# Performance work log

Measured on AMD Instinct MI355X. Metric: run time of the kernel, lower is better.

The kernel has to match this reference:

```python
import jax, jax.numpy as jnp
import numpy as np

# dims (match init_kwargs)
L, D, H, K = 8, 384, 6, 64            # layers, hidden, rwkv heads, rwkv head dim
DI, MH, HD, DS, CK = 768, 12, 64, 64, 4  # mamba: d_inner, heads, head_dim, d_state, conv kernel
V, B, T = 32000, 1, 1024


def _rms(x, w, eps=1e-6):
    return w * x * jax.lax.rsqrt(jnp.mean(x * x, axis=-1, keepdims=True) + eps)


def _rwkv6(xn, Wr, Wk, Wv, Wg, Ww, w_bias, u, gn_w, gn_b, Wo):
    # RWKV6: data-dependent diagonal-decay linear attention
    Bb, Tt, Dd = xn.shape
    proj = lambda W: (xn @ W).reshape(Bb, Tt, H, K)
    r, k, v = proj(Wr), proj(Wk), proj(Wv)
    g = xn @ Wg                                        # [B,T,D]
    w = (xn @ Ww + w_bias).reshape(Bb, Tt, H, K)
    decay = jnp.exp(-jnp.exp(w))                       # in (0,1)

    def step(S, inp):                                  # S: [B,H,K,K] (key x value)
        r_t, k_t, v_t, d_t = inp                       # each [B,H,K]
        kv = k_t[..., :, None] * v_t[..., None, :]     # [B,H,K,K]
        o = jnp.einsum('bhk,bhkv->bhv', r_t, S + u[None, :, :, None] * kv)
        S = d_t[..., None] * S + kv
        return S, o

    tm = lambda a: jnp.moveaxis(a, 1, 0)               # time-major
    S0 = jnp.zeros((Bb, H, K, K), xn.dtype)
    _, o = jax.lax.scan(step, S0, (tm(r), tm(k), tm(v), tm(decay)))
    o = jnp.moveaxis(o, 0, 1)                          # [B,T,H,K]
    # per-head GroupNorm
    mu = jnp.mean(o, -1, keepdims=True)
    var = jnp.var(o, -1, keepdims=True)
    o = (o - mu) * jax.lax.rsqrt(var + 1e-5) * gn_w.reshape(H, K) + gn_b.reshape(H, K)
    o = o.reshape(Bb, Tt, Dd) * jax.nn.silu(g)
    return o @ Wo


def _mamba2(xn, W_in, conv_w, conv_b, dt_bias, A_log, Dp, mn_w, W_out):
    # Mamba2: selective scan with scalar A per head
    Bb, Tt, Dd = xn.shape
    zxbcdt = xn @ W_in                                 # [B,T, 2*DI + 2*DS + MH]
    z = zxbcdt[..., :DI]
    xBC = zxbcdt[..., DI:DI + DI + 2 * DS]
    dt = jax.nn.softplus(zxbcdt[..., -MH:] + dt_bias)  # [B,T,MH]
    # causal depthwise conv1d, kernel CK
    xp = jnp.pad(xBC, ((0, 0), (CK - 1, 0), (0, 0)))
    xBC = sum(xp[:, j:j + Tt, :] * conv_w[:, j] for j in range(CK)) + conv_b
    xBC = jax.nn.silu(xBC)
    xs = xBC[..., :DI].reshape(Bb, Tt, MH, HD)
    Bm = xBC[..., DI:DI + DS]                          # [B,T,DS]
    Cm = xBC[..., DI + DS:]                            # [B,T,DS]
    A = -jnp.exp(A_log)                                # [MH]

    def step(S, inp):                                  # S: [B,MH,HD,DS]
        x_t, B_t, C_t, dt_t = inp                      # [B,MH,HD],[B,DS],[B,DS],[B,MH]
        dA = jnp.exp(dt_t * A)                         # [B,MH]
        S = dA[..., None, None] * S + (dt_t[..., None] * x_t)[..., None] * B_t[:, None, None, :]
        y = jnp.einsum('bhps,bs->bhp', S, C_t) + Dp[None, :, None] * x_t
        return S, y

    tm = lambda a: jnp.moveaxis(a, 1, 0)
    S0 = jnp.zeros((Bb, MH, HD, DS), xn.dtype)
    _, y = jax.lax.scan(step, S0, (tm(xs), tm(Bm), tm(Cm), tm(dt)))
    y = jnp.moveaxis(y, 0, 1).reshape(Bb, Tt, DI)
    y = _rms(y * jax.nn.silu(z), mn_w)                 # gated RMSNorm
    return y @ W_out


def _forward(x, embed, ln_w, Wr, Wk, Wv, Wg, Ww, w_bias, u, gn_w, gn_b, Wo,
             W_in, conv_w, conv_b, dt_bias, A_log, Dp, mn_w, W_out,
             gw, gb, ffn_ln_w, ffn_w1, ffn_w2, ln_out_w):
    h = jnp.take(embed, x, axis=0)                     # [B,T,D]
    for i in range(L):
        xn = _rms(h, ln_w[i])
        o_r = _rwkv6(xn, Wr[i], Wk[i], Wv[i], Wg[i], Ww[i], w_bias[i], u[i], gn_w[i], gn_b[i], Wo[i])
        o_m = _mamba2(xn, W_in[i], conv_w[i], conv_b[i], dt_bias[i], A_log[i], Dp[i], mn_w[i], W_out[i])
        gate = jax.nn.sigmoid(jnp.concatenate([o_r, o_m], -1) @ gw[i] + gb[i])  # [B,T,1]
        h = h + gate * o_r + (1.0 - gate) * o_m
        hn = _rms(h, ffn_ln_w[i])
        h = h + jax.nn.gelu(hn @ ffn_w1[i], approximate=False) @ ffn_w2[i]
    h = _rms(h, ln_out_w)
    return h @ embed.T                                 # tied head -> [B,T,V]


def setup_inputs() -> dict:
    key = jax.random.key(0)
    ks = iter(jax.random.split(key, 32))
    n = lambda shape, s=0.02: jax.random.normal(next(ks), shape, jnp.float32) * s
    d = {}
    d['x'] = jax.random.randint(next(ks), (B, T), 0, V)
    d['embed'] = n((V, D))
    d['ln_w'] = jnp.ones((L, D), jnp.float32)
    d['Wr'] = n((L, D, D)); d['Wk'] = n((L, D, D)); d['Wv'] = n((L, D, D))
    d['Wg'] = n((L, D, D)); d['Ww'] = n((L, D, D))
    d['w_bias'] = n((L, D), 0.5)
    d['u'] = n((L, H, K), 0.5)
    d['gn_w'] = jnp.ones((L, D), jnp.float32)
    d['gn_b'] = jnp.zeros((L, D), jnp.float32)
    d['Wo'] = n((L, D, D))
    d['W_in'] = n((L, D, 2 * DI + 2 * DS + MH))
    d['conv_w'] = n((L, DI + 2 * DS, CK), 0.2)
    d['conv_b'] = jnp.zeros((L, DI + 2 * DS), jnp.float32)
    d['dt_bias'] = jax.random.uniform(next(ks), (L, MH), jnp.float32, -4.0, -1.0)
    d['A_log'] = jnp.log(jax.random.uniform(next(ks), (L, MH), jnp.float32, 1.0, 16.0))
    d['Dp'] = jnp.ones((L, MH), jnp.float32)
    d['mn_w'] = jnp.ones((L, DI), jnp.float32)
    d['W_out'] = n((L, DI, D))
    d['gw'] = n((L, 2 * D, 1), 0.01)
    d['gb'] = jnp.full((L, 1), float(np.log(0.3 / 0.7)), jnp.float32)
    d['ffn_ln_w'] = jnp.ones((L, D), jnp.float32)
    d['ffn_w1'] = n((L, D, 4 * D))
    d['ffn_w2'] = n((L, 4 * D, D))
    d['ln_out_w'] = jnp.ones((D,), jnp.float32)
    return d


def reference(x, embed, ln_w, Wr, Wk, Wv, Wg, Ww, w_bias, u, gn_w, gn_b, Wo,
              W_in, conv_w, conv_b, dt_bias, A_log, Dp, mn_w, W_out,
              gw, gb, ffn_ln_w, ffn_w1, ffn_w2, ln_out_w):
    return _forward(x, embed, ln_w, Wr, Wk, Wv, Wg, Ww, w_bias, u, gn_w, gn_b, Wo,
                    W_in, conv_w, conv_b, dt_bias, A_log, Dp, mn_w, W_out,
                    gw, gb, ffn_ln_w, ffn_w1, ffn_w2, ln_out_w)
```

## Files before the change

kernel.cpp:

```cpp
#include <hip/hip_runtime.h>
#include <math.h>

#define TT 1024
#define DD 384
#define NH 6
#define DI 768
#define MH 12
#define DS 64
#define NL 8
#define XDIM 1676
#define CONVC 896
#define NV 32000
#define PZS 3712
#define G_OFF 1152
#define W_OFF 1536
#define Z_OFF 1920
#define XBC_OFF 2688
#define DT_OFF 3584
#define CHK 32
#define NCH 32

typedef __attribute__((ext_vector_type(8))) short short8;
typedef __attribute__((ext_vector_type(4))) float f32x4;

__device__ __forceinline__ float siluf(float x) { return x / (1.f + expf(-x)); }
__device__ __forceinline__ float sigmoidf_(float x) { return 1.f / (1.f + expf(-x)); }
__device__ __forceinline__ float geluf(float x) {
  return 0.5f * x * (1.f + erff(x * 0.70710678118654752440f));
}
__device__ __forceinline__ unsigned short f2b(float x) {
  union { float f; unsigned int u; } v; v.f = x;
  unsigned int r = v.u + 0x7fffu + ((v.u >> 16) & 1u);
  return (unsigned short)(r >> 16);
}

#define GLDS(gp, lp) __builtin_amdgcn_global_load_lds( \
    (const __attribute__((address_space(1))) void*)(gp), \
    (__attribute__((address_space(3))) void*)(lp), 16, 0, 0)

template<int EPI>
__global__ __launch_bounds__(256) void gemm_bf16(
    const unsigned short* __restrict__ A, const unsigned short* __restrict__ Bt,
    float* __restrict__ C, unsigned short* __restrict__ Cb, int N, int K, int ldC)
{
  __shared__ unsigned short As[2048];
  __shared__ unsigned short Bs[2048];
  int tid = threadIdx.x;
  int wid = tid >> 6, lane = tid & 63;
  int m0 = blockIdx.y * 64, n0 = blockIdx.x * 64;
  int wr = wid >> 1, wc = wid & 1;
  int sr = tid >> 2;
  int scs = ((tid & 3) ^ ((sr >> 1) & 3)) * 8;
  const unsigned short* ga = A  + (size_t)(m0 + sr) * K + scs;
  const unsigned short* gb = Bt + (size_t)(n0 + sr) * K + scs;
  unsigned short* la = As + wid * 512;
  unsigned short* lb = Bs + wid * 512;
  int fr = lane & 15, fc = lane >> 4;
  f32x4 zz = {0.f, 0.f, 0.f, 0.f};
  f32x4 acc[2][2];
  acc[0][0] = zz; acc[0][1] = zz; acc[1][0] = zz; acc[1][1] = zz;

  int kper = K / (int)gridDim.z;
  int ks = blockIdx.z * kper, ke = ks + kper;
  for (int k0 = ks; k0 < ke; k0 += 32) {
    GLDS(ga + k0, la);
    GLDS(gb + k0, lb);
    __syncthreads();
    short8 af[2], bf[2];
#pragma unroll
    for (int mg = 0; mg < 2; ++mg) {
      int ar = wr * 32 + mg * 16 + fr;
      af[mg] = *reinterpret_cast<const short8*>(&As[ar * 32 + ((fc ^ ((ar >> 1) & 3)) * 8)]);
    }
#pragma unroll
    for (int ng = 0; ng < 2; ++ng) {
      int br = wc * 32 + ng * 16 + fr;
      bf[ng] = *reinterpret_cast<const short8*>(&Bs[br * 32 + ((fc ^ ((br >> 1) & 3)) * 8)]);
    }
#pragma unroll
    for (int mg = 0; mg < 2; ++mg)
#pragma unroll
      for (int ng = 0; ng < 2; ++ng)
        acc[mg][ng] = __builtin_amdgcn_mfma_f32_16x16x32_bf16(af[mg], bf[ng], acc[mg][ng], 0, 0, 0);
    __syncthreads();
  }
#pragma unroll
  for (int mg = 0; mg < 2; ++mg)
#pragma unroll
    for (int ng = 0; ng < 2; ++ng) {
      int col = n0 + wc * 32 + ng * 16 + fr;
      if (col < N) {
#pragma unroll
        for (int j = 0; j < 4; ++j) {
          int row = m0 + wr * 32 + mg * 16 + fc * 4 + j;
          if (EPI == 1)      Cb[(size_t)row * ldC + col] = f2b(geluf(acc[mg][ng][j]));
          else if (EPI == 3) atomicAdd(&C[(size_t)row * ldC + col], acc[mg][ng][j]);
          else               C[(size_t)row * ldC + col]  = acc[mg][ng][j];
        }
      }
    }
}

__global__ __launch_bounds__(256) void gemm_dual(
    const unsigned short* __restrict__ A0, const unsigned short* __restrict__ B0t,
    float* __restrict__ C0, int K0, int ld0, int nx0, int nb0,
    const unsigned short* __restrict__ A1, const unsigned short* __restrict__ B1t,
    float* __restrict__ C1, int K1, int ld1, int nx1)
{
  __shared__ unsigned short As[2048];
  __shared__ unsigned short Bs[2048];
  int b = blockIdx.x;
  const unsigned short *A, *Bt; float* C; int K, ldC, bx, by;
  if (b < nb0) { A = A0; Bt = B0t; C = C0; K = K0; ldC = ld0; bx = b % nx0; by = b / nx0; }
  else { b -= nb0; A = A1; Bt = B1t; C = C1; K = K1; ldC = ld1; bx = b % nx1; by = b / nx1; }
  int tid = threadIdx.x;
  int wid = tid >> 6, lane = tid & 63;
  int m0 = by * 64, n0 = bx * 64;
  int wr = wid >> 1, wc = wid & 1;
  int sr = tid >> 2;
  int scs = ((tid & 3) ^ ((sr >> 1) & 3)) * 8;
  const unsigned short* ga = A  + (size_t)(m0 + sr) * K + scs;
  const unsigned short* gb = Bt + (size_t)(n0 + sr) * K + scs;
  unsigned short* la = As + wid * 512;
  unsigned short* lb = Bs + wid * 512;
  int fr = lane & 15, fc = lane >> 4;
  f32x4 zz = {0.f, 0.f, 0.f, 0.f};
  f32x4 acc[2][2];
  acc[0][0] = zz; acc[0][1] = zz; acc[1][0] = zz; acc[1][1] = zz;
  for (int k0 = 0; k0 < K; k0 += 32) {
    GLDS(ga + k0, la);
    GLDS(gb + k0, lb);
    __syncthreads();
    short8 af[2], bf[2];
#pragma unroll
    for (int mg = 0; mg < 2; ++mg) {
      int ar = wr * 32 + mg * 16 + fr;
      af[mg] = *reinterpret_cast<const short8*>(&As[ar * 32 + ((fc ^ ((ar >> 1) & 3)) * 8)]);
    }
#pragma unroll
    for (int ng = 0; ng < 2; ++ng) {
      int br = wc * 32 + ng * 16 + fr;
      bf[ng] = *reinterpret_cast<const short8*>(&Bs[br * 32 + ((fc ^ ((br >> 1) & 3)) * 8)]);
    }
#pragma unroll
    for (int mg = 0; mg < 2; ++mg)
#pragma unroll
      for (int ng = 0; ng < 2; ++ng)
        acc[mg][ng] = __builtin_amdgcn_mfma_f32_16x16x32_bf16(af[mg], bf[ng], acc[mg][ng], 0, 0, 0);
    __syncthreads();
  }
#pragma unroll
  for (int mg = 0; mg < 2; ++mg)
#pragma unroll
    for (int ng = 0; ng < 2; ++ng) {
      int col = n0 + wc * 32 + ng * 16 + fr;
#pragma unroll
      for (int j = 0; j < 4; ++j) {
        int row = m0 + wr * 32 + mg * 16 + fc * 4 + j;
        C[(size_t)row * ldC + col] = acc[mg][ng][j];
      }
    }
}

__global__ __launch_bounds__(256) void gemm128(
    const unsigned short* __restrict__ A, const unsigned short* __restrict__ Bt,
    float* __restrict__ C, int N, int K, int ldC)
{
  __shared__ unsigned short As[4096];
  __shared__ unsigned short Bs[4096];
  int tid = threadIdx.x;
  int wid = tid >> 6, lane = tid & 63;
  int m0 = blockIdx.y * 128, n0 = blockIdx.x * 128;
  int wr = wid >> 1, wc = wid & 1;
  int r0 = tid >> 2;
  int scs = ((tid & 3) ^ ((r0 >> 1) & 3)) * 8;
  const unsigned short* ga0 = A  + (size_t)(m0 + r0) * K + scs;
  const unsigned short* gb0 = Bt + (size_t)(n0 + r0) * K + scs;
  const unsigned short* ga1 = ga0 + (size_t)64 * K;
  const unsigned short* gb1 = gb0 + (size_t)64 * K;
  unsigned short* la0 = As + wid * 512;
  unsigned short* lb0 = Bs + wid * 512;
  unsigned short* la1 = As + 2048 + wid * 512;
  unsigned short* lb1 = Bs + 2048 + wid * 512;
  int fr = lane & 15, fc = lane >> 4;
  f32x4 zz = {0.f, 0.f, 0.f, 0.f};
  f32x4 acc[4][4];
#pragma unroll
  for (int i = 0; i < 4; i++)
#pragma unroll
    for (int j = 0; j < 4; j++) acc[i][j] = zz;

  for (int k0 = 0; k0 < K; k0 += 32) {
    GLDS(ga0 + k0, la0);
    GLDS(gb0 + k0, lb0);
    GLDS(ga1 + k0, la1);
    GLDS(gb1 + k0, lb1);
    __syncthreads();
    short8 af[4], bf[4];
#pragma unroll
    for (int mg = 0; mg < 4; ++mg) {
      int ar = wr * 64 + mg * 16 + fr;
      af[mg] = *reinterpret_cast<const short8*>(&As[ar * 32 + ((fc ^ ((ar >> 1) & 3)) * 8)]);
    }
#pragma unroll
    for (int ng = 0; ng < 4; ++ng) {
      int br = wc * 64 + ng * 16 + fr;
      bf[ng] = *reinterpret_cast<const short8*>(&Bs[br * 32 + ((fc ^ ((br >> 1) & 3)) * 8)]);
    }
#pragma unroll
    for (int mg = 0; mg < 4; ++mg)
#pragma unroll
      for (int ng = 0; ng < 4; ++ng)
        acc[mg][ng] = __builtin_amdgcn_mfma_f32_16x16x32_bf16(af[mg], bf[ng], acc[mg][ng], 0, 0, 0);
    __syncthreads();
  }
#pragma unroll
  for (int mg = 0; mg < 4; ++mg)
#pragma unroll
    for (int ng = 0; ng < 4; ++ng) {
      int col = n0 + wc * 64 + ng * 16 + fr;
      if (col < N) {
#pragma unroll
        for (int j = 0; j < 4; ++j) {
          int row = m0 + wr * 64 + mg * 16 + fc * 4 + j;
          C[(size_t)row * ldC + col] = acc[mg][ng][j];
        }
      }
    }
}

__global__ __launch_bounds__(256) void transconv_kernel(
    const float* __restrict__ src, unsigned short* __restrict__ dst,
    int K, int N, int Npad, size_t srcStride, size_t dstStride)
{
  __shared__ float tile[32][33];
  src += (size_t)blockIdx.z * srcStride;
  dst += (size_t)blockIdx.z * dstStride;
  int k0 = blockIdx.y * 32, n0 = blockIdx.x * 32;
  int tx = threadIdx.x & 31, ty = threadIdx.x >> 5;
  for (int i = ty; i < 32; i += 8) {
    int k = k0 + i, n = n0 + tx;
    tile[i][tx] = (k < K && n < N) ? src[(size_t)k * N + n] : 0.f;
  }
  __syncthreads();
  for (int i = ty; i < 32; i += 8) {
    int n = n0 + i, k = k0 + tx;
    if (n < Npad && k < K) dst[(size_t)n * K + k] = f2b(tile[tx][i]);
  }
}

__global__ void conv_b16_kernel(const float* __restrict__ src, unsigned short* __restrict__ dst, int n)
{
  int idx = blockIdx.x * 256 + threadIdx.x;
  if (idx < n) dst[idx] = f2b(src[idx]);
}

__global__ void embed_kernel(const int* __restrict__ x, const float* __restrict__ embed,
                             float* __restrict__ h)
{
  int idx = blockIdx.x * 256 + threadIdx.x;
  if (idx < TT * DD) {
    int t = idx / DD, d = idx % DD;
    h[idx] = embed[(size_t)x[t] * DD + d];
  }
}

__global__ __launch_bounds__(256) void rms_kernel(const float* __restrict__ in,
                                                  const float* __restrict__ w,
                                                  unsigned short* __restrict__ out)
{
  int row = blockIdx.x * 4 + (threadIdx.x >> 6);
  int lane = threadIdx.x & 63;
  const float* r = in + (size_t)row * DD;
  float v[6]; float ss = 0.f;
#pragma unroll
  for (int j = 0; j < 6; ++j) { v[j] = r[lane + j * 64]; ss = fmaf(v[j], v[j], ss); }
#pragma unroll
  for (int s = 1; s < 64; s <<= 1) ss += __shfl_xor(ss, s);
  float scale = rsqrtf(ss * (1.f / DD) + 1e-6f);
#pragma unroll
  for (int j = 0; j < 6; ++j)
    out[(size_t)row * DD + lane + j * 64] = f2b(w[lane + j * 64] * v[j] * scale);
}

__global__ __launch_bounds__(256) void scanA_kernel(
    const float* __restrict__ PZ, const float* __restrict__ u, const float* __restrict__ wbias,
    float* __restrict__ so, float* __restrict__ rPb,
    float* __restrict__ MstR, float* __restrict__ DcR,
    const float* __restrict__ cw, const float* __restrict__ cbia,
    const float* __restrict__ dtbias,
    const float* __restrict__ Alog, const float* __restrict__ Dpw,
    float* __restrict__ yb, float* __restrict__ Ccb,
    float* __restrict__ MstM, float* __restrict__ DcM)
{
  __shared__ float smem[2 * 256 + 64];
  int b = blockIdx.x, tid = threadIdx.x;
  if (b < 192) {
    int h = b >> 5, c = b & 31;
    float* sbuf = smem; float* us = smem + 512;
    if (tid < 64) us[tid] = u[h * 64 + tid];
    int wv = tid >> 6, l = tid & 63;
    int vv = wv * 16 + (l & 15);
    int kc = l >> 4;
    int arr = tid >> 6, idx = tid & 63;
    int off = (arr == 0) ? 0 : (arr == 1) ? 384 : (arr == 2) ? W_OFF : 768;
    float wb = (arr == 2) ? wbias[h * 64 + idx] : 0.f;
    size_t base = (size_t)h * 64 + idx + off;
    int t0 = c * CHK;
    float S[16], Pc[16];
#pragma unroll
    for (int i = 0; i < 16; i++) { S[i] = 0.f; Pc[i] = 1.f; }
    float reg = PZ[(size_t)t0 * PZS + base];
    bool st = (wv == 0) && ((l & 15) == 0);
    for (int t = 0; t < CHK; ++t) {
      int tt = t0 + t;
      float* cb = sbuf + (t & 1) * 256;
      cb[arr * 64 + idx] = (arr == 2) ? expf(-expf(reg + wb)) : reg;
      if (t + 1 < CHK) reg = PZ[(size_t)(tt + 1) * PZS + base];
      __syncthreads();
      float vt = cb[192 + vv];
      float acc = 0.f;
      float rp[16];
#pragma unroll
      for (int i = 0; i < 16; ++i) {
        int kk = kc * 16 + i;
        float rv = cb[kk], kv = cb[64 + kk], dv = cb[128 + kk];
        rp[i] = rv * Pc[i];
        float kvv = kv * vt;
        acc = fmaf(rv, fmaf(us[kk], kvv, S[i]), acc);
        S[i] = fmaf(dv, S[i], kvv);
        Pc[i] *= dv;
      }
      acc += __shfl_xor(acc, 16);
      acc += __shfl_xor(acc, 32);
      if (l < 16) so[(size_t)tt * DD + h * 64 + vv] = acc;
      if (st) {
        float4* dst = (float4*)&rPb[(size_t)tt * DD + h * 64 + kc * 16];
        dst[0] = make_float4(rp[0], rp[1], rp[2], rp[3]);
        dst[1] = make_float4(rp[4], rp[5], rp[6], rp[7]);
        dst[2] = make_float4(rp[8], rp[9], rp[10], rp[11]);
        dst[3] = make_float4(rp[12], rp[13], rp[14], rp[15]);
      }
    }
    float* ms = MstR + (size_t)(h * NCH + c) * 4096;
    float4* msv = (float4*)&ms[vv * 64 + kc * 16];
    msv[0] = make_float4(S[0], S[1], S[2], S[3]);
    msv[1] = make_float4(S[4], S[5], S[6], S[7]);
    msv[2] = make_float4(S[8], S[9], S[10], S[11]);
    msv[3] = make_float4(S[12], S[13], S[14], S[15]);
    if (st) {
      float4* dd_ = (float4*)&DcR[(h * NCH + c) * 64 + kc * 16];
      dd_[0] = make_float4(Pc[0], Pc[1], Pc[2], Pc[3]);
      dd_[1] = make_float4(Pc[4], Pc[5], Pc[6], Pc[7]);
      dd_[2] = make_float4(Pc[8], Pc[9], Pc[10], Pc[11]);
      dd_[3] = make_float4(Pc[12], Pc[13], Pc[14], Pc[15]);
    }
  } else {
    int bb = b - 192;
    int hh = bb >> 5, c = bb & 31;
    float* sbuf = smem;
    int wv = tid >> 6, l = tid & 63;
    int p = wv * 16 + (l & 15);
    int sc = l >> 4;
    int arr = tid >> 6, idx = tid & 63;
    float A = -expf(Alog[hh]);
    float Dph = Dpw[hh];
    float dtbh = dtbias[hh];
    int t0 = c * CHK;
    float cw0 = 0.f, cw1 = 0.f, cw2 = 0.f, cw3 = 0.f, cbv = 0.f;
    float xw0 = 0.f, xw1 = 0.f, xw2 = 0.f, cur = 0.f;
    const float* xcol = nullptr;
    float reg = 0.f;
    if (arr < 3) {
      int ch = (arr == 0) ? (hh * 64 + idx) : (arr == 1) ? (DI + idx) : (DI + DS + idx);
      cw0 = cw[ch * 4 + 0]; cw1 = cw[ch * 4 + 1]; cw2 = cw[ch * 4 + 2]; cw3 = cw[ch * 4 + 3];
      cbv = cbia[ch];
      xcol = PZ + XBC_OFF + ch;
      xw0 = (t0 >= 3) ? xcol[(size_t)(t0 - 3) * PZS] : 0.f;
      xw1 = (t0 >= 2) ? xcol[(size_t)(t0 - 2) * PZS] : 0.f;
      xw2 = (t0 >= 1) ? xcol[(size_t)(t0 - 1) * PZS] : 0.f;
      cur = xcol[(size_t)t0 * PZS];
    } else {
      reg = PZ[(size_t)t0 * PZS + DT_OFF + hh];
    }
    float S[16]; float cdA = 1.f;
#pragma unroll
    for (int i = 0; i < 16; i++) S[i] = 0.f;
    bool st = (wv == 0) && ((l & 15) == 0);
    for (int t = 0; t < CHK; ++t) {
      int tt = t0 + t;
      float* cb = sbuf + (t & 1) * 256;
      if (arr < 3) {
        float cvv = fmaf(cw3, cur, fmaf(cw2, xw2, fmaf(cw1, xw1, fmaf(cw0, xw0, cbv))));
        cb[arr * 64 + idx] = siluf(cvv);
        float nx = (t + 1 < CHK) ? xcol[(size_t)(tt + 1) * PZS] : 0.f;
        xw0 = xw1; xw1 = xw2; xw2 = cur; cur = nx;
      } else {
        if (idx == 0) {
          float v = reg + dtbh;
          cb[192] = (v > 20.f) ? v : log1pf(expf(v));
        }
        if (t + 1 < CHK) reg = PZ[(size_t)(tt + 1) * PZS + DT_OFF + hh];
      }
      __syncthreads();
      float dt_ = cb[192];
      float dA = expf(dt_ * A);
      cdA *= dA;
      float xp = cb[p];
      float dtx = dt_ * xp;
      float acc = 0.f;
#pragma unroll
      for (int i = 0; i < 16; ++i) {
        int s = sc * 16 + i;
        S[i] = fmaf(dA, S[i], dtx * cb[64 + s]);
        acc = fmaf(S[i], cb[128 + s], acc);
      }
      acc += __shfl_xor(acc, 16);
      acc += __shfl_xor(acc, 32);
      if (l < 16) yb[(size_t)tt * DI + hh * 64 + p] = fmaf(Dph, xp, acc);
      if (st) {
        float4* dst = (float4*)&Ccb[(size_t)tt * DI + hh * 64 + sc * 16];
#pragma unroll
        for (int j4 = 0; j4 < 4; ++j4)
          dst[j4] = make_float4(cdA * cb[128 + sc * 16 + j4 * 4 + 0],
                                cdA * cb[128 + sc * 16 + j4 * 4 + 1],
                                cdA * cb[128 + sc * 16 + j4 * 4 + 2],
                                cdA * cb[128 + sc * 16 + j4 * 4 + 3]);
      }
    }
    float* ms = MstM + (size_t)(hh * NCH + c) * 4096;
    float4* msv = (float4*)&ms[p * 64 + sc * 16];
    msv[0] = make_float4(S[0], S[1], S[2], S[3]);
    msv[1] = make_float4(S[4], S[5], S[6], S[7]);
    msv[2] = make_float4(S[8], S[9], S[10], S[11]);
    msv[3] = make_float4(S[12], S[13], S[14], S[15]);
    if (tid == 0) DcM[hh * NCH + c] = cdA;
  }
}

__global__ __launch_bounds__(256) void combine_kernel(
    const float* __restrict__ MstR, const float* __restrict__ DcR, float* __restrict__ S0R,
    const float* __restrict__ MstM, const float* __restrict__ DcM, float* __restrict__ S0M)
{
  int b = blockIdx.x, tid = threadIdx.x;
  if (b < 96) {
    int h = b >> 4, sub = b & 15;
    int ei = sub * 256 + tid;
    int k = ei & 63;
    float S = 0.f;
#pragma unroll
    for (int c = 0; c < NCH; ++c) {
      size_t base = (size_t)(h * NCH + c) * 4096;
      float m = MstR[base + ei];
      float dD = DcR[(h * NCH + c) * 64 + k];
      S0R[base + ei] = S;
      S = fmaf(dD, S, m);
    }
  } else {
    int bb = b - 96;
    int hh = bb >> 4, sub = bb & 15;
    int ei = sub * 256 + tid;
    float S = 0.f;
#pragma unroll
    for (int c = 0; c < NCH; ++c) {
      size_t base = (size_t)(hh * NCH + c) * 4096;
      float m = MstM[base + ei];
      float dD = DcM[hh * NCH + c];
      S0M[base + ei] = S;
      S = fmaf(dD, S, m);
    }
  }
}

__global__ __launch_bounds__(256) void corr_kernel(
    const float* __restrict__ S0R, const float* __restrict__ rPb, const float* __restrict__ so,
    const float* __restrict__ S0M, const float* __restrict__ Ccb, float* __restrict__ yb,
    const float* __restrict__ PZ, const float* __restrict__ gnw, const float* __restrict__ gnb,
    unsigned short* __restrict__ gob)
{
  __shared__ float S0l[64 * 68];
  __shared__ float Rl[CHK * 68];
  int b = blockIdx.x, tid = threadIdx.x;
  const float* s0g; const float* rg; int ostride, obase, t0;
  bool rwkv = (b < 192);
  int h;
  if (rwkv) {
    h = b >> 5; int c = b & 31; t0 = c * CHK;
    s0g = S0R + (size_t)(h * NCH + c) * 4096;
    rg = rPb; obase = h * 64; ostride = DD;
  } else {
    int bb = b - 192; h = bb >> 5; int c = bb & 31; t0 = c * CHK;
    s0g = S0M + (size_t)(h * NCH + c) * 4096;
    rg = Ccb; obase = h * 64; ostride = DI;
  }
  for (int gi = tid; gi < 4096; gi += 256)
    S0l[(gi & 63) * 68 + (gi >> 6)] = s0g[gi];
  {
    int t = tid >> 3, q = (tid & 7) * 8;
    const float4* src = (const float4*)&rg[(size_t)(t0 + t) * ostride + obase + q];
    float4* dst = (float4*)&Rl[t * 68 + q];
    dst[0] = src[0]; dst[1] = src[1];
  }
  __syncthreads();
  int t = tid >> 3, q = (tid & 7) * 8;
  float acc[8];
#pragma unroll
  for (int j = 0; j < 8; j++) acc[j] = 0.f;
  for (int k = 0; k < 64; ++k) {
    float rv = Rl[t * 68 + k];
    const float4* sp = (const float4*)&S0l[k * 68 + q];
    float4 s0 = sp[0], s1 = sp[1];
    acc[0] = fmaf(rv, s0.x, acc[0]);
    acc[1] = fmaf(rv, s0.y, acc[1]);
    acc[2] = fmaf(rv, s0.z, acc[2]);
    acc[3] = fmaf(rv, s0.w, acc[3]);
    acc[4] = fmaf(rv, s1.x, acc[4]);
    acc[5] = fmaf(rv, s1.y, acc[5]);
    acc[6] = fmaf(rv, s1.z, acc[6]);
    acc[7] = fmaf(rv, s1.w, acc[7]);
  }
  if (!rwkv) {
    float4* op = (float4*)&yb[(size_t)(t0 + t) * DI + obase + q];
    float4 c0 = op[0], c1 = op[1];
    c0.x += acc[0]; c0.y += acc[1]; c0.z += acc[2]; c0.w += acc[3];
    c1.x += acc[4]; c1.y += acc[5]; c1.z += acc[6]; c1.w += acc[7];
    op[0] = c0; op[1] = c1;
  } else {
    float ov[8];
    const float4* sp = (const float4*)&so[(size_t)(t0 + t) * DD + obase + q];
    float4 s0 = sp[0], s1 = sp[1];
    ov[0] = s0.x + acc[0]; ov[1] = s0.y + acc[1]; ov[2] = s0.z + acc[2]; ov[3] = s0.w + acc[3];
    ov[4] = s1.x + acc[4]; ov[5] = s1.y + acc[5]; ov[6] = s1.z + acc[6]; ov[7] = s1.w + acc[7];
    float m_ = 0.f;
#pragma unroll
    for (int j = 0; j < 8; j++) m_ += ov[j];
    m_ += __shfl_xor(m_, 1); m_ += __shfl_xor(m_, 2); m_ += __shfl_xor(m_, 4);
    float mu = m_ * (1.f / 64.f);
    float vv = 0.f;
#pragma unroll
    for (int j = 0; j < 8; j++) { float d = ov[j] - mu; vv = fmaf(d, d, vv); }
    vv += __shfl_xor(vv, 1); vv += __shfl_xor(vv, 2); vv += __shfl_xor(vv, 4);
    float rstd = rsqrtf(vv * (1.f / 64.f) + 1e-5f);
#pragma unroll
    for (int j = 0; j < 8; j++) {
      int d = obase + q + j;
      float gv = PZ[(size_t)(t0 + t) * PZS + G_OFF + d];
      float o = fmaf((ov[j] - mu) * rstd, gnw[d], gnb[d]) * siluf(gv);
      gob[(size_t)(t0 + t) * DD + d] = f2b(o);
    }
  }
}

__global__ __launch_bounds__(256) void mamba_norm_kernel(const float* __restrict__ yb,
    const float* __restrict__ PZ, const float* __restrict__ mnw, unsigned short* __restrict__ out)
{
  int row = blockIdx.x * 4 + (threadIdx.x >> 6);
  int lane = threadIdx.x & 63;
  float v[12]; float ss = 0.f;
#pragma unroll
  for (int j = 0; j < 12; ++j) {
    int c = lane + j * 64;
    float z = PZ[(size_t)row * PZS + Z_OFF + c];
    float t = yb[(size_t)row * DI + c] * siluf(z);
    v[j] = t; ss = fmaf(t, t, ss);
  }
#pragma unroll
  for (int s = 1; s < 64; s <<= 1) ss += __shfl_xor(ss, s);
  float scale = rsqrtf(ss * (1.f / DI) + 1e-6f);
#pragma unroll
  for (int j = 0; j < 12; ++j) {
    int c = lane + j * 64;
    out[(size_t)row * DI + c] = f2b(v[j] * scale * mnw[c]);
  }
}

__global__ __launch_bounds__(256) void gate_rms_kernel(const float* __restrict__ orb,
    const float* __restrict__ omb, const float* __restrict__ gw,
    const float* __restrict__ gb, const float* __restrict__ flnw,
    float* __restrict__ h, unsigned short* __restrict__ xnb)
{
  int row = blockIdx.x * 4 + (threadIdx.x >> 6);
  int lane = threadIdx.x & 63;
  float a[6], bq[6]; float ss = 0.f;
#pragma unroll
  for (int j = 0; j < 6; ++j) {
    int c = lane + j * 64;
    a[j] = orb[(size_t)row * DD + c]; bq[j] = omb[(size_t)row * DD + c];
    ss += a[j] * gw[c] + bq[j] * gw[DD + c];
  }
#pragma unroll
  for (int s = 1; s < 64; s <<= 1) ss += __shfl_xor(ss, s);
  float gate = sigmoidf_(ss + gb[0]);
  float hn[6]; float ss2 = 0.f;
#pragma unroll
  for (int j = 0; j < 6; ++j) {
    int c = lane + j * 64;
    size_t ix = (size_t)row * DD + c;
    hn[j] = h[ix] + gate * a[j] + (1.f - gate) * bq[j];
    h[ix] = hn[j];
    ss2 = fmaf(hn[j], hn[j], ss2);
  }
#pragma unroll
  for (int s = 1; s < 64; s <<= 1) ss2 += __shfl_xor(ss2, s);
  float scale = rsqrtf(ss2 * (1.f / DD) + 1e-6f);
#pragma unroll
  for (int j = 0; j < 6; ++j) {
    int c = lane + j * 64;
    xnb[(size_t)row * DD + c] = f2b(flnw[c] * hn[j] * scale);
  }
}

extern "C" void kernel_launch(void* const* d_in, const int* in_sizes, int n_in,
                              void* d_out, int out_size, void* d_ws, size_t ws_size,
                              hipStream_t stream)
{
  const int*   x        = (const int*)  d_in[0];
  const float* embed    = (const float*)d_in[1];
  const float* ln_w     = (const float*)d_in[2];
  const float* Wr       = (const float*)d_in[3];
  const float* Wk       = (const float*)d_in[4];
  const float* Wv       = (const float*)d_in[5];
  const float* Wg       = (const float*)d_in[6];
  const float* Ww       = (const float*)d_in[7];
  const float* w_bias   = (const float*)d_in[8];
  const float* u        = (const float*)d_in[9];
  const float* gn_w     = (const float*)d_in[10];
  const float* gn_b     = (const float*)d_in[11];
  const float* Wo       = (const float*)d_in[12];
  const float* W_in     = (const float*)d_in[13];
  const float* conv_w   = (const float*)d_in[14];
  const float* conv_b   = (const float*)d_in[15];
  const float* dt_bias  = (const float*)d_in[16];
  const float* A_log    = (const float*)d_in[17];
  const float* Dp       = (const float*)d_in[18];
  const float* mn_w     = (const float*)d_in[19];
  const float* W_out    = (const float*)d_in[20];
  const float* gw       = (const float*)d_in[21];
  const float* gb       = (const float*)d_in[22];
  const float* ffn_ln_w = (const float*)d_in[23];
  const float* ffn_w1   = (const float*)d_in[24];
  const float* ffn_w2   = (const float*)d_in[25];
  const float* ln_out_w = (const float*)d_in[26];

  char* base = (char*)d_ws;
  size_t off = 0;
  auto alloc = [&](size_t bytes) { off = (off + 255) & ~(size_t)255; void* p = base + off; off += bytes; return p; };

  float* h    = (float*)alloc((size_t)TT * DD * 4);
  float* PZ   = (float*)alloc((size_t)TT * PZS * 4);
  float* yb   = (float*)alloc((size_t)TT * DI * 4);
  float* so   = (float*)alloc((size_t)TT * DD * 4);
  float* orb  = (float*)alloc((size_t)TT * DD * 4);
  float* omb  = (float*)alloc((size_t)TT * DD * 4);
  float* rPb  = (float*)alloc((size_t)TT * DD * 4);
  float* Ccb  = (float*)alloc((size_t)TT * DI * 4);
  float* MstR = (float*)alloc((size_t)NH * NCH * 4096 * 4);
  float* DcR  = (float*)alloc((size_t)NH * NCH * 64 * 4);
  float* S0R  = (float*)alloc((size_t)NH * NCH * 4096 * 4);
  float* MstM = (float*)alloc((size_t)MH * NCH * 4096 * 4);
  float* DcM  = (float*)alloc((size_t)MH * NCH * 4);
  float* S0M  = (float*)alloc((size_t)MH * NCH * 4096 * 4);
  unsigned short* xnb = (unsigned short*)alloc((size_t)TT * DD * 2);
  unsigned short* gob = (unsigned short*)alloc((size_t)TT * DD * 2);
  unsigned short* ynb = (unsigned short*)alloc((size_t)TT * DI * 2);
  unsigned short* fhb = (unsigned short*)alloc((size_t)TT * 1536 * 2);
  unsigned short* WallT = (unsigned short*)alloc((size_t)NL * PZS * 384 * 2);
  unsigned short* WoT   = (unsigned short*)alloc((size_t)NL * 384 * 384 * 2);
  unsigned short* WoutT = (unsigned short*)alloc((size_t)NL * 384 * 768 * 2);
  unsigned short* F1T   = (unsigned short*)alloc((size_t)NL * 1536 * 384 * 2);
  unsigned short* F2T   = (unsigned short*)alloc((size_t)NL * 384 * 1536 * 2);
  unsigned short* embB  = (unsigned short*)alloc((size_t)NV * DD * 2);
  (void)ws_size; (void)in_sizes; (void)n_in; (void)out_size;

  dim3 blk(256);
  int gTD = (TT * DD + 255) / 256;

  const float* Wrkvgw[5] = {Wr, Wk, Wv, Wg, Ww};
  for (int j = 0; j < 5; ++j)
    transconv_kernel<<<dim3(12, 12, 8), blk, 0, stream>>>(
        Wrkvgw[j], WallT + (size_t)j * 384 * 384, 384, 384, 384,
        (size_t)384 * 384, (size_t)PZS * 384);
  transconv_kernel<<<dim3(56, 12, 8), blk, 0, stream>>>(
      W_in, WallT + (size_t)1920 * 384, 384, XDIM, 1792,
      (size_t)384 * XDIM, (size_t)PZS * 384);
  transconv_kernel<<<dim3(12, 12, 8), blk, 0, stream>>>(
      Wo, WoT, 384, 384, 384, (size_t)384 * 384, (size_t)384 * 384);
  transconv_kernel<<<dim3(12, 24, 8), blk, 0, stream>>>(
      W_out, WoutT, 768, 384, 384, (size_t)768 * 384, (size_t)384 * 768);
  transconv_kernel<<<dim3(48, 12, 8), blk, 0, stream>>>(
      ffn_w1, F1T, 384, 1536, 1536, (size_t)384 * 1536, (size_t)1536 * 384);
  transconv_kernel<<<dim3(12, 48, 8), blk, 0, stream>>>(
      ffn_w2, F2T, 1536, 384, 384, (size_t)1536 * 384, (size_t)384 * 1536);
  conv_b16_kernel<<<(NV * DD + 255) / 256, blk, 0, stream>>>(embed, embB, NV * DD);

  embed_kernel<<<gTD, blk, 0, stream>>>(x, embed, h);

  for (int i = 0; i < NL; ++i) {
    rms_kernel<<<256, blk, 0, stream>>>(h, ln_w + (size_t)i * DD, xnb);

    gemm_bf16<0><<<dim3(58, 16), blk, 0, stream>>>(
        xnb, WallT + (size_t)i * PZS * 384, PZ, nullptr, PZS, 384, PZS);

    scanA_kernel<<<576, blk, 0, stream>>>(PZ, u + (size_t)i * NH * 64, w_bias + (size_t)i * DD,
                                          so, rPb, MstR, DcR,
                                          conv_w + (size_t)i * CONVC * 4, conv_b + (size_t)i * CONVC,
                                          dt_bias + (size_t)i * MH,
                                          A_log + (size_t)i * MH, Dp + (size_t)i * MH,
                                          yb, Ccb, MstM, DcM);
    combine_kernel<<<288, blk, 0, stream>>>(MstR, DcR, S0R, MstM, DcM, S0M);
    corr_kernel<<<576, blk, 0, stream>>>(S0R, rPb, so, S0M, Ccb, yb,
                                         PZ, gn_w + (size_t)i * DD, gn_b + (size_t)i * DD, gob);

    mamba_norm_kernel<<<256, blk, 0, stream>>>(yb, PZ, mn_w + (size_t)i * DI, ynb);

    gemm_dual<<<192, blk, 0, stream>>>(
        gob, WoT + (size_t)i * 384 * 384, orb, 384, DD, 6, 96,
        ynb, WoutT + (size_t)i * 384 * 768, omb, 768, DD, 6);

    gate_rms_kernel<<<256, blk, 0, stream>>>(orb, omb, gw + (size_t)i * 2 * DD, gb + i,
                                             ffn_ln_w + (size_t)i * DD, h, xnb);

    gemm_bf16<1><<<dim3(24, 16), blk, 0, stream>>>(
        xnb, F1T + (size_t)i * 1536 * 384, nullptr, fhb, 1536, 384, 1536);
    gemm_bf16<3><<<dim3(6, 16, 4), blk, 0, stream>>>(
        fhb, F2T + (size_t)i * 384 * 1536, h, nullptr, DD, 1536, DD);
  }

  rms_kernel<<<256, blk, 0, stream>>>(h, ln_out_w, xnb);
  gemm128<<<dim3(250, 8), blk, 0, stream>>>(
      xnb, embB, (float*)d_out, NV, 384, NV);
}
```

Measured before the change: 980.6 us.

## Double GEMM K-step, batch weight transposes, fold chunk-state combine into correction

All three GEMM kernels now stage 64-wide K tiles (two MFMA sub-steps per barrier) with an 8-way XOR swizzle, halving the number of loop iterations and barriers. The ten weight transpose/convert launches are merged into a single table-driven launch. The separate combine kernel is removed: each correction block recomputes its own prefix chunk state in registers by looping over prior chunks. This drops one launch per layer and two scratch buffers, but later chunks redo up to 31 chunk-state reads, so the correction kernel does redundant global traffic.

```diff
diff --git a/kernel.cpp b/kernel.cpp
--- a/kernel.cpp
+++ b/kernel.cpp
@@ -43,16 +43,16 @@
     const unsigned short* __restrict__ A, const unsigned short* __restrict__ Bt,
     float* __restrict__ C, unsigned short* __restrict__ Cb, int N, int K, int ldC)
 {
-  __shared__ unsigned short As[2048];
-  __shared__ unsigned short Bs[2048];
+  __shared__ unsigned short As[4096];
+  __shared__ unsigned short Bs[4096];
   int tid = threadIdx.x;
   int wid = tid >> 6, lane = tid & 63;
   int m0 = blockIdx.y * 64, n0 = blockIdx.x * 64;
   int wr = wid >> 1, wc = wid & 1;
-  int sr = tid >> 2;
-  int scs = ((tid & 3) ^ ((sr >> 1) & 3)) * 8;
-  const unsigned short* ga = A  + (size_t)(m0 + sr) * K + scs;
-  const unsigned short* gb = Bt + (size_t)(n0 + sr) * K + scs;
+  int r0 = tid >> 3, ch = tid & 7;
+  int scs = (ch ^ (r0 & 7)) * 8;
+  const unsigned short* ga = A  + (size_t)(m0 + r0) * K + scs;
+  const unsigned short* gb = Bt + (size_t)(n0 + r0) * K + scs;
   unsigned short* la = As + wid * 512;
   unsigned short* lb = Bs + wid * 512;
   int fr = lane & 15, fc = lane >> 4;
@@ -62,26 +62,32 @@
 
   int kper = K / (int)gridDim.z;
   int ks = blockIdx.z * kper, ke = ks + kper;
-  for (int k0 = ks; k0 < ke; k0 += 32) {
+  size_t row32 = (size_t)32 * K;
+  for (int k0 = ks; k0 < ke; k0 += 64) {
     GLDS(ga + k0, la);
+    GLDS(ga + k0 + row32, la + 2048);
     GLDS(gb + k0, lb);
+    GLDS(gb + k0 + row32, lb + 2048);
     __syncthreads();
-    short8 af[2], bf[2];
-#pragma unroll
-    for (int mg = 0; mg < 2; ++mg) {
-      int ar = wr * 32 + mg * 16 + fr;
-      af[mg] = *reinterpret_cast<const short8*>(&As[ar * 32 + ((fc ^ ((ar >> 1) & 3)) * 8)]);
-    }
-#pragma unroll
-    for (int ng = 0; ng < 2; ++ng) {
-      int br = wc * 32 + ng * 16 + fr;
-      bf[ng] = *reinterpret_cast<const short8*>(&Bs[br * 32 + ((fc ^ ((br >> 1) & 3)) * 8)]);
-    }
-#pragma unroll
-    for (int mg = 0; mg < 2; ++mg)
-#pragma unroll
-      for (int ng = 0; ng < 2; ++ng)
-        acc[mg][ng] = __builtin_amdgcn_mfma_f32_16x16x32_bf16(af[mg], bf[ng], acc[mg][ng], 0, 0, 0);
+#pragma unroll
+    for (int kh = 0; kh < 2; ++kh) {
+      short8 af[2], bf[2];
+#pragma unroll
+      for (int mg = 0; mg < 2; ++mg) {
+        int ar = wr * 32 + mg * 16 + fr;
+        af[mg] = *reinterpret_cast<const short8*>(&As[ar * 64 + (((kh * 4 + fc) ^ (ar & 7)) * 8)]);
+      }
+#pragma unroll
+      for (int ng = 0; ng < 2; ++ng) {
+        int br = wc * 32 + ng * 16 + fr;
+        bf[ng] = *reinterpret_cast<const short8*>(&Bs[br * 64 + (((kh * 4 + fc) ^ (br & 7)) * 8)]);
+      }
+#pragma unroll
+      for (int mg = 0; mg < 2; ++mg)
+#pragma unroll
+        for (int ng = 0; ng < 2; ++ng)
+          acc[mg][ng] = __builtin_amdgcn_mfma_f32_16x16x32_bf16(af[mg], bf[ng], acc[mg][ng], 0, 0, 0);
+    }
     __syncthreads();
   }
 #pragma unroll
@@ -107,8 +113,8 @@
     const unsigned short* __restrict__ A1, const unsigned short* __restrict__ B1t,
     float* __restrict__ C1, int K1, int ld1, int nx1)
 {
-  __shared__ unsigned short As[2048];
-  __shared__ unsigned short Bs[2048];
+  __shared__ unsigned short As[4096];
+  __shared__ unsigned short Bs[4096];
   int b = blockIdx.x;
   const unsigned short *A, *Bt; float* C; int K, ldC, bx, by;
   if (b < nb0) { A = A0; Bt = B0t; C = C0; K = K0; ldC = ld0; bx = b % nx0; by = b / nx0; }
@@ -117,36 +123,42 @@
   int wid = tid >> 6, lane = tid & 63;
   int m0 = by * 64, n0 = bx * 64;
   int wr = wid >> 1, wc = wid & 1;
-  int sr = tid >> 2;
-  int scs = ((tid & 3) ^ ((sr >> 1) & 3)) * 8;
-  const unsigned short* ga = A  + (size_t)(m0 + sr) * K + scs;
-  const unsigned short* gb = Bt + (size_t)(n0 + sr) * K + scs;
+  int r0 = tid >> 3, ch = tid & 7;
+  int scs = (ch ^ (r0 & 7)) * 8;
+  const unsigned short* ga = A  + (size_t)(m0 + r0) * K + scs;
+  const unsigned short* gb = Bt + (size_t)(n0 + r0) * K + scs;
   unsigned short* la = As + wid * 512;
   unsigned short* lb = Bs + wid * 512;
   int fr = lane & 15, fc = lane >> 4;
   f32x4 zz = {0.f, 0.f, 0.f, 0.f};
   f32x4 acc[2][2];
   acc[0][0] = zz; acc[0][1] = zz; acc[1][0] = zz; acc[1][1] = zz;
-  for (int k0 = 0; k0 < K; k0 += 32) {
+  size_t row32 = (size_t)32 * K;
+  for (int k0 = 0; k0 < K; k0 += 64) {
     GLDS(ga + k0, la);
+    GLDS(ga + k0 + row32, la + 2048);
     GLDS(gb + k0, lb);
+    GLDS(gb + k0 + row32, lb + 2048);
     __syncthreads();
-    short8 af[2], bf[2];
-#pragma unroll
-    for (int mg = 0; mg < 2; ++mg) {
-      int ar = wr * 32 + mg * 16 + fr;
-      af[mg] = *reinterpret_cast<const short8*>(&As[ar * 32 + ((fc ^ ((ar >> 1) & 3)) * 8)]);
-    }
-#pragma unroll
-    for (int ng = 0; ng < 2; ++ng) {
-      int br = wc * 32 + ng * 16 + fr;
-      bf[ng] = *reinterpret_cast<const short8*>(&Bs[br * 32 + ((fc ^ ((br >> 1) & 3)) * 8)]);
-    }
-#pragma unroll
-    for (int mg = 0; mg < 2; ++mg)
-#pragma unroll
-      for (int ng = 0; ng < 2; ++ng)
-        acc[mg][ng] = __builtin_amdgcn_mfma_f32_16x16x32_bf16(af[mg], bf[ng], acc[mg][ng], 0, 0, 0);
+#pragma unroll
+    for (int kh = 0; kh < 2; ++kh) {
+      short8 af[2], bf[2];
+#pragma unroll
+      for (int mg = 0; mg < 2; ++mg) {
+        int ar = wr * 32 + mg * 16 + fr;
+        af[mg] = *reinterpret_cast<const short8*>(&As[ar * 64 + (((kh * 4 + fc) ^ (ar & 7)) * 8)]);
+      }
+#pragma unroll
+      for (int ng = 0; ng < 2; ++ng) {
+        int br = wc * 32 + ng * 16 + fr;
+        bf[ng] = *reinterpret_cast<const short8*>(&Bs[br * 64 + (((kh * 4 + fc) ^ (br & 7)) * 8)]);
+      }
+#pragma unroll
+      for (int mg = 0; mg < 2; ++mg)
+#pragma unroll
+        for (int ng = 0; ng < 2; ++ng)
+          acc[mg][ng] = __builtin_amdgcn_mfma_f32_16x16x32_bf16(af[mg], bf[ng], acc[mg][ng], 0, 0, 0);
+    }
     __syncthreads();
   }
 #pragma unroll
@@ -166,22 +178,16 @@
     const unsigned short* __restrict__ A, const unsigned short* __restrict__ Bt,
     float* __restrict__ C, int N, int K, int ldC)
 {
-  __shared__ unsigned short As[4096];
-  __shared__ unsigned short Bs[4096];
+  __shared__ unsigned short As[8192];
+  __shared__ unsigned short Bs[8192];
   int tid = threadIdx.x;
   int wid = tid >> 6, lane = tid & 63;
   int m0 = blockIdx.y * 128, n0 = blockIdx.x * 128;
   int wr = wid >> 1, wc = wid & 1;
-  int r0 = tid >> 2;
-  int scs = ((tid & 3) ^ ((r0 >> 1) & 3)) * 8;
-  const unsigned short* ga0 = A  + (size_t)(m0 + r0) * K + scs;
-  const unsigned short* gb0 = Bt + (size_t)(n0 + r0) * K + scs;
-  const unsigned short* ga1 = ga0 + (size_t)64 * K;
-  const unsigned short* gb1 = gb0 + (size_t)64 * K;
-  unsigned short* la0 = As + wid * 512;
-  unsigned short* lb0 = Bs + wid * 512;
-  unsigned short* la1 = As + 2048 + wid * 512;
-  unsigned short* lb1 = Bs + 2048 + wid * 512;
+  int r0 = tid >> 3, ch = tid & 7;
+  int scs = (ch ^ (r0 & 7)) * 8;
+  const unsigned short* ga = A  + (size_t)(m0 + r0) * K + scs;
+  const unsigned short* gb = Bt + (size_t)(n0 + r0) * K + scs;
   int fr = lane & 15, fc = lane >> 4;
   f32x4 zz = {0.f, 0.f, 0.f, 0.f};
   f32x4 acc[4][4];
@@ -190,28 +196,33 @@
 #pragma unroll
     for (int j = 0; j < 4; j++) acc[i][j] = zz;
 
-  for (int k0 = 0; k0 < K; k0 += 32) {
-    GLDS(ga0 + k0, la0);
-    GLDS(gb0 + k0, lb0);
-    GLDS(ga1 + k0, la1);
-    GLDS(gb1 + k0, lb1);
+  size_t row32 = (size_t)32 * K;
+  for (int k0 = 0; k0 < K; k0 += 64) {
+#pragma unroll
+    for (int i = 0; i < 4; ++i) {
+      GLDS(ga + k0 + i * row32, As + i * 2048 + wid * 512);
+      GLDS(gb + k0 + i * row32, Bs + i * 2048 + wid * 512);
+    }
     __syncthreads();
-    short8 af[4], bf[4];
-#pragma unroll
-    for (int mg = 0; mg < 4; ++mg) {
-      int ar = wr * 64 + mg * 16 + fr;
-      af[mg] = *reinterpret_cast<const short8*>(&As[ar * 32 + ((fc ^ ((ar >> 1) & 3)) * 8)]);
-    }
-#pragma unroll
-    for (int ng = 0; ng < 4; ++ng) {
-      int br = wc * 64 + ng * 16 + fr;
-      bf[ng] = *reinterpret_cast<const short8*>(&Bs[br * 32 + ((fc ^ ((br >> 1) & 3)) * 8)]);
-    }
-#pragma unroll
-    for (int mg = 0; mg < 4; ++mg)
-#pragma unroll
-      for (int ng = 0; ng < 4; ++ng)
-        acc[mg][ng] = __builtin_amdgcn_mfma_f32_16x16x32_bf16(af[mg], bf[ng], acc[mg][ng], 0, 0, 0);
+#pragma unroll
+    for (int kh = 0; kh < 2; ++kh) {
+      short8 af[4], bf[4];
+#pragma unroll
+      for (int mg = 0; mg < 4; ++mg) {
+        int ar = wr * 64 + mg * 16 + fr;
+        af[mg] = *reinterpret_cast<const short8*>(&As[ar * 64 + (((kh * 4 + fc) ^ (ar & 7)) * 8)]);
+      }
+#pragma unroll
+      for (int ng = 0; ng < 4; ++ng) {
+        int br = wc * 64 + ng * 16 + fr;
+        bf[ng] = *reinterpret_cast<const short8*>(&Bs[br * 64 + (((kh * 4 + fc) ^ (br & 7)) * 8)]);
+      }
+#pragma unroll
+      for (int mg = 0; mg < 4; ++mg)
+#pragma unroll
+        for (int ng = 0; ng < 4; ++ng)
+          acc[mg][ng] = __builtin_amdgcn_mfma_f32_16x16x32_bf16(af[mg], bf[ng], acc[mg][ng], 0, 0, 0);
+    }
     __syncthreads();
   }
 #pragma unroll
@@ -229,23 +240,31 @@
     }
 }
 
-__global__ __launch_bounds__(256) void transconv_kernel(
-    const float* __restrict__ src, unsigned short* __restrict__ dst,
-    int K, int N, int Npad, size_t srcStride, size_t dstStride)
+struct TCJob { const float* src; unsigned short* dst; int K, N, Npad, nx; size_t sStr, dStr; int tend; };
+struct TC10 { TCJob j[10]; };
+
+__global__ __launch_bounds__(256) void transconv_all(TC10 P)
 {
   __shared__ float tile[32][33];
-  src += (size_t)blockIdx.z * srcStride;
-  dst += (size_t)blockIdx.z * dstStride;
-  int k0 = blockIdx.y * 32, n0 = blockIdx.x * 32;
+  int bid = blockIdx.x;
+  int q = 0;
+  while (bid >= P.j[q].tend) ++q;
+  int tstart = (q == 0) ? 0 : P.j[q - 1].tend;
+  TCJob jb = P.j[q];
+  int local = bid - tstart;
+  int bx = local % jb.nx, by = local / jb.nx;
+  const float* src = jb.src + (size_t)blockIdx.y * jb.sStr;
+  unsigned short* dst = jb.dst + (size_t)blockIdx.y * jb.dStr;
+  int k0 = by * 32, n0 = bx * 32;
   int tx = threadIdx.x & 31, ty = threadIdx.x >> 5;
   for (int i = ty; i < 32; i += 8) {
     int k = k0 + i, n = n0 + tx;
-    tile[i][tx] = (k < K && n < N) ? src[(size_t)k * N + n] : 0.f;
+    tile[i][tx] = (k < jb.K && n < jb.N) ? src[(size_t)k * jb.N + n] : 0.f;
   }
   __syncthreads();
   for (int i = ty; i < 32; i += 8) {
     int n = n0 + i, k = k0 + tx;
-    if (n < Npad && k < K) dst[(size_t)n * K + k] = f2b(tile[tx][i]);
+    if (n < jb.Npad && k < jb.K) dst[(size_t)n * jb.K + k] = f2b(tile[tx][i]);
   }
 }
 
@@ -372,10 +391,10 @@
     const float* xcol = nullptr;
     float reg = 0.f;
     if (arr < 3) {
-      int ch = (arr == 0) ? (hh * 64 + idx) : (arr == 1) ? (DI + idx) : (DI + DS + idx);
-      cw0 = cw[ch * 4 + 0]; cw1 = cw[ch * 4 + 1]; cw2 = cw[ch * 4 + 2]; cw3 = cw[ch * 4 + 3];
-      cbv = cbia[ch];
-      xcol = PZ + XBC_OFF + ch;
+      int chn = (arr == 0) ? (hh * 64 + idx) : (arr == 1) ? (DI + idx) : (DI + DS + idx);
+      cw0 = cw[chn * 4 + 0]; cw1 = cw[chn * 4 + 1]; cw2 = cw[chn * 4 + 2]; cw3 = cw[chn * 4 + 3];
+      cbv = cbia[chn];
+      xcol = PZ + XBC_OFF + chn;
       xw0 = (t0 >= 3) ? xcol[(size_t)(t0 - 3) * PZS] : 0.f;
       xw1 = (t0 >= 2) ? xcol[(size_t)(t0 - 2) * PZS] : 0.f;
       xw2 = (t0 >= 1) ? xcol[(size_t)(t0 - 1) * PZS] : 0.f;
@@ -438,63 +457,54 @@
   }
 }
 
-__global__ __launch_bounds__(256) void combine_kernel(
-    const float* __restrict__ MstR, const float* __restrict__ DcR, float* __restrict__ S0R,
-    const float* __restrict__ MstM, const float* __restrict__ DcM, float* __restrict__ S0M)
-{
-  int b = blockIdx.x, tid = threadIdx.x;
-  if (b < 96) {
-    int h = b >> 4, sub = b & 15;
-    int ei = sub * 256 + tid;
-    int k = ei & 63;
-    float S = 0.f;
-#pragma unroll
-    for (int c = 0; c < NCH; ++c) {
-      size_t base = (size_t)(h * NCH + c) * 4096;
-      float m = MstR[base + ei];
-      float dD = DcR[(h * NCH + c) * 64 + k];
-      S0R[base + ei] = S;
-      S = fmaf(dD, S, m);
-    }
-  } else {
-    int bb = b - 96;
-    int hh = bb >> 4, sub = bb & 15;
-    int ei = sub * 256 + tid;
-    float S = 0.f;
-#pragma unroll
-    for (int c = 0; c < NCH; ++c) {
-      size_t base = (size_t)(hh * NCH + c) * 4096;
-      float m = MstM[base + ei];
-      float dD = DcM[hh * NCH + c];
-      S0M[base + ei] = S;
-      S = fmaf(dD, S, m);
-    }
-  }
-}
-
 __global__ __launch_bounds__(256) void corr_kernel(
-    const float* __restrict__ S0R, const float* __restrict__ rPb, const float* __restrict__ so,
-    const float* __restrict__ S0M, const float* __restrict__ Ccb, float* __restrict__ yb,
+    const float* __restrict__ MstR, const float* __restrict__ DcR,
+    const float* __restrict__ rPb, const float* __restrict__ so,
+    const float* __restrict__ MstM, const float* __restrict__ DcM,
+    const float* __restrict__ Ccb, float* __restrict__ yb,
     const float* __restrict__ PZ, const float* __restrict__ gnw, const float* __restrict__ gnb,
     unsigned short* __restrict__ gob)
 {
   __shared__ float S0l[64 * 68];
   __shared__ float Rl[CHK * 68];
   int b = blockIdx.x, tid = threadIdx.x;
-  const float* s0g; const float* rg; int ostride, obase, t0;
+  const float* rg; int ostride, obase, t0;
   bool rwkv = (b < 192);
-  int h;
+  int h, cidx;
   if (rwkv) {
-    h = b >> 5; int c = b & 31; t0 = c * CHK;
-    s0g = S0R + (size_t)(h * NCH + c) * 4096;
+    h = b >> 5; cidx = b & 31;
     rg = rPb; obase = h * 64; ostride = DD;
   } else {
-    int bb = b - 192; h = bb >> 5; int c = bb & 31; t0 = c * CHK;
-    s0g = S0M + (size_t)(h * NCH + c) * 4096;
+    int bb = b - 192; h = bb >> 5; cidx = bb & 31;
     rg = Ccb; obase = h * 64; ostride = DI;
   }
-  for (int gi = tid; gi < 4096; gi += 256)
-    S0l[(gi & 63) * 68 + (gi >> 6)] = s0g[gi];
+  t0 = cidx * CHK;
+  float Sreg[16];
+#pragma unroll
+  for (int it = 0; it < 16; ++it) Sreg[it] = 0.f;
+  if (rwkv) {
+    int kk = tid & 63;
+    for (int cp = 0; cp < cidx; ++cp) {
+      float d = DcR[(h * NCH + cp) * 64 + kk];
+      const float* mb = MstR + (size_t)(h * NCH + cp) * 4096;
+#pragma unroll
+      for (int it = 0; it < 16; ++it)
+        Sreg[it] = fmaf(d, Sreg[it], mb[tid + 256 * it]);
+    }
+  } else {
+    for (int cp = 0; cp < cidx; ++cp) {
+      float d = DcM[h * NCH + cp];
+      const float* mb = MstM + (size_t)(h * NCH + cp) * 4096;
+#pragma unroll
+      for (int it = 0; it < 16; ++it)
+        Sreg[it] = fmaf(d, Sreg[it], mb[tid + 256 * it]);
+    }
+  }
+#pragma unroll
+  for (int it = 0; it < 16; ++it) {
+    int gi = tid + 256 * it;
+    S0l[(gi & 63) * 68 + (gi >> 6)] = Sreg[it];
+  }
   {
     int t = tid >> 3, q = (tid & 7) * 8;
     const float4* src = (const float4*)&rg[(size_t)(t0 + t) * ostride + obase + q];
@@ -656,10 +666,8 @@
   float* Ccb  = (float*)alloc((size_t)TT * DI * 4);
   float* MstR = (float*)alloc((size_t)NH * NCH * 4096 * 4);
   float* DcR  = (float*)alloc((size_t)NH * NCH * 64 * 4);
-  float* S0R  = (float*)alloc((size_t)NH * NCH * 4096 * 4);
   float* MstM = (float*)alloc((size_t)MH * NCH * 4096 * 4);
   float* DcM  = (float*)alloc((size_t)MH * NCH * 4);
-  float* S0M  = (float*)alloc((size_t)MH * NCH * 4096 * 4);
   unsigned short* xnb = (unsigned short*)alloc((size_t)TT * DD * 2);
   unsigned short* gob = (unsigned short*)alloc((size_t)TT * DD * 2);
   unsigned short* ynb = (unsigned short*)alloc((size_t)TT * DI * 2);
@@ -675,24 +683,25 @@
   dim3 blk(256);
   int gTD = (TT * DD + 255) / 256;
 
-  const float* Wrkvgw[5] = {Wr, Wk, Wv, Wg, Ww};
-  for (int j = 0; j < 5; ++j)
-    transconv_kernel<<<dim3(12, 12, 8), blk, 0, stream>>>(
-        Wrkvgw[j], WallT + (size_t)j * 384 * 384, 384, 384, 384,
-        (size_t)384 * 384, (size_t)PZS * 384);
-  transconv_kernel<<<dim3(56, 12, 8), blk, 0, stream>>>(
-      W_in, WallT + (size_t)1920 * 384, 384, XDIM, 1792,
-      (size_t)384 * XDIM, (size_t)PZS * 384);
-  transconv_kernel<<<dim3(12, 12, 8), blk, 0, stream>>>(
-      Wo, WoT, 384, 384, 384, (size_t)384 * 384, (size_t)384 * 384);
-  transconv_kernel<<<dim3(12, 24, 8), blk, 0, stream>>>(
-      W_out, WoutT, 768, 384, 384, (size_t)768 * 384, (size_t)384 * 768);
-  transconv_kernel<<<dim3(48, 12, 8), blk, 0, stream>>>(
-      ffn_w1, F1T, 384, 1536, 1536, (size_t)384 * 1536, (size_t)1536 * 384);
-  transconv_kernel<<<dim3(12, 48, 8), blk, 0, stream>>>(
-      ffn_w2, F2T, 1536, 384, 384, (size_t)1536 * 384, (size_t)384 * 1536);
+  TC10 tc;
+  int te = 0;
+  auto setjob = [&](int q, const float* src, unsigned short* dst, int K, int N, int Npad,
+                    int nx, int ny, size_t sStr, size_t dStr) {
+    te += nx * ny;
+    tc.j[q] = TCJob{src, dst, K, N, Npad, nx, sStr, dStr, te};
+  };
+  setjob(0, Wr, WallT + (size_t)0 * 384 * 384, 384, 384, 384, 12, 12, (size_t)384 * 384, (size_t)PZS * 384);
+  setjob(1, Wk, WallT + (size_t)1 * 384 * 384, 384, 384, 384, 12, 12, (size_t)384 * 384, (size_t)PZS * 384);
+  setjob(2, Wv, WallT + (size_t)2 * 384 * 384, 384, 384, 384, 12, 12, (size_t)384 * 384, (size_t)PZS * 384);
+  setjob(3, Wg, WallT + (size_t)3 * 384 * 384, 384, 384, 384, 12, 12, (size_t)384 * 384, (size_t)PZS * 384);
+  setjob(4, Ww, WallT + (size_t)4 * 384 * 384, 384, 384, 384, 12, 12, (size_t)384 * 384, (size_t)PZS * 384);
+  setjob(5, W_in, WallT + (size_t)1920 * 384, 384, XDIM, 1792, 56, 12, (size_t)384 * XDIM, (size_t)PZS * 384);
+  setjob(6, Wo, WoT, 384, 384, 384, 12, 12, (size_t)384 * 384, (size_t)384 * 384);
+  setjob(7, W_out, WoutT, 768, 384, 384, 12, 24, (size_t)768 * 384, (size_t)384 * 768);
+  setjob(8, ffn_w1, F1T, 384, 1536, 1536, 48, 12, (size_t)384 * 1536, (size_t)1536 * 384);
+  setjob(9, ffn_w2, F2T, 1536, 384, 384, 12, 48, (size_t)1536 * 384, (size_t)384 * 1536);
+  transconv_all<<<dim3(te, 8), blk, 0, stream>>>(tc);
   conv_b16_kernel<<<(NV * DD + 255) / 256, blk, 0, stream>>>(embed, embB, NV * DD);
-
   embed_kernel<<<gTD, blk, 0, stream>>>(x, embed, h);
 
   for (int i = 0; i < NL; ++i) {
@@ -707,8 +716,7 @@
                                           dt_bias + (size_t)i * MH,
                                           A_log + (size_t)i * MH, Dp + (size_t)i * MH,
                                           yb, Ccb, MstM, DcM);
-    combine_kernel<<<288, blk, 0, stream>>>(MstR, DcR, S0R, MstM, DcM, S0M);
-    corr_kernel<<<576, blk, 0, stream>>>(S0R, rPb, so, S0M, Ccb, yb,
+    corr_kernel<<<576, blk, 0, stream>>>(MstR, DcR, rPb, so, MstM, DcM, Ccb, yb,
                                          PZ, gn_w + (size_t)i * DD, gn_b + (size_t)i * DD, gob);
 
     mamba_norm_kernel<<<256, blk, 0, stream>>>(yb, PZ, mn_w + (size_t)i * DI, ynb);
```

Result: no change. 983.0 us (+0.2%).
